# Optimization experiments

Hardware: AMD Instinct MI355X
Metric: run time of the kernel (lower is better)

## Reference

```python
import jax, jax.numpy as jnp
import numpy as np

ALPHA = 0.2          # LeakyReLU negative slope
ORTHO_LAMBDA = 0.01  # orthogonal regularization weight


def setup_inputs() -> dict:
    key = jax.random.key(0)
    ks = jax.random.split(key, 9)
    N, IN, OUT, NR, H = 50000, 128, 128, 64, 4
    E1, E2 = 200000, 50000
    return {
        "input": jax.random.normal(ks[0], (N, IN), jnp.float32),
        "edge": jax.random.randint(ks[1], (2, E1), 0, N),
        "edge_embed": jax.random.normal(ks[2], (E1, NR), jnp.float32),
        "edge_list_nhop": jax.random.randint(ks[3], (2, E2), 0, N),
        "edge_embed_nhop": jax.random.normal(ks[4], (E2, NR), jnp.float32),
        "proj": jax.random.normal(ks[5], (H, IN, IN), jnp.float32) / np.sqrt(IN).astype(np.float32),
        "W": jax.random.normal(ks[6], (H, OUT, 2 * IN + NR), jnp.float32) * 0.08,
        "a": jax.random.normal(ks[7], (H, 1, OUT), jnp.float32) * 0.1,
        "head_weights": jnp.ones((H,), jnp.float32),
    }


def reference(input, edge, edge_embed, edge_list_nhop, edge_embed_nhop, proj, W, a, head_weights):
    N, IN = input.shape
    H, OUT, _ = W.shape
    e = jnp.concatenate([edge, edge_list_nhop], axis=1)              # [2, E]
    emb = jnp.concatenate([edge_embed, edge_embed_nhop], axis=0)     # [E, NR]
    src, tgt = e[0], e[1]

    # per-head orthogonal projections: head_input[h] = input @ proj[h].T -> [H, N, IN]
    hin = jnp.einsum('ni,hoi->hno', input, proj)

    # edge_m = W @ concat(h_src, h_tgt, rel) without materializing the concat
    W_src, W_tgt, W_rel = W[:, :, :IN], W[:, :, IN:2 * IN], W[:, :, 2 * IN:]
    edge_m = (jnp.einsum('hei,hoi->heo', hin[:, src, :], W_src)
              + jnp.einsum('hei,hoi->heo', hin[:, tgt, :], W_tgt)
              + jnp.einsum('er,hor->heo', emb, W_rel))               # [H, E, OUT]

    scores = jnp.einsum('heo,ho->he', edge_m, a[:, 0, :])            # [H, E]
    powers = -jnp.where(scores > 0, scores, ALPHA * scores)         # -leakyrelu
    edge_e = jnp.exp(powers)                                         # [H, E]

    seg = lambda v: jax.ops.segment_sum(v, src, num_segments=N)
    e_rowsum = jnp.clip(jax.vmap(seg)(edge_e), 1e-12, None)          # [H, N]

    edge_w = edge_e[:, :, None] * edge_m                             # [H, E, OUT]
    head_out = jax.vmap(seg)(edge_w)                                 # [H, N, OUT]

    w = jax.nn.softmax(head_weights)
    out = jnp.einsum('h,hnd->nd', w, head_out)                       # [N, OUT]
    # faithful to torch: divides by the LAST head's e_rowsum (loop leakage)
    out = out / e_rowsum[-1][:, None]

    pp = jnp.einsum('hij,hkj->hik', proj, proj)                      # proj @ proj.T
    eye = jnp.eye(proj.shape[1], dtype=proj.dtype)
    orth_reg = ORTHO_LAMBDA * jnp.sum(jnp.sqrt(jnp.sum((pp - eye) ** 2, axis=(1, 2))))

    return jax.nn.elu(out), orth_reg
```

## Files before the change

kernel.cpp:

```cpp
#include <hip/hip_runtime.h>
#include <math.h>


#define NHEAD 4

typedef unsigned short u16;
typedef __attribute__((ext_vector_type(4))) unsigned short u16x4;
typedef __attribute__((ext_vector_type(8))) unsigned short u16x8;
typedef __attribute__((ext_vector_type(8))) short bf16x8;
typedef __attribute__((ext_vector_type(4))) float f32x4;

__device__ __forceinline__ float bf2f(u16 v) {
    union { unsigned u; float f; } x; x.u = ((unsigned)v) << 16; return x.f;
}
__device__ __forceinline__ u16 f2bf(float f) {
    union { float f; unsigned u; } x; x.f = f;
    const unsigned r = x.u + 0x7FFFu + ((x.u >> 16) & 1u);
    return (u16)(r >> 16);
}

__global__ __launch_bounds__(256) void k1_prep(
    const float* __restrict__ proj, const float* __restrict__ W,
    const float* __restrict__ a, const float* __restrict__ hw,
    u16* __restrict__ M_bf,
    float* __restrict__ asrc, float* __restrict__ atgt, float* __restrict__ arel,
    u16* __restrict__ WcatT_bf, float* __restrict__ wsoft,
    float* __restrict__ orth_part)
{
    __shared__ float projS[128*132];
    __shared__ float WS[32*132];
    __shared__ float tS[128];
    __shared__ float red[256];
    const int h = blockIdx.x;
    const int part = blockIdx.y;
    const int z = blockIdx.z;
    const int tid = threadIdx.x;
    if (part < 2 && z >= 4) return;
    const float* projH = proj + h*(128*128);
    const float* WH = W + h*(128*320);
    const float* aH = a + h*128;

    {
        const float4* p4 = (const float4*)projH;
        for (int idx = tid; idx < 4096; idx += 256)
            *(float4*)&projS[(idx>>5)*132 + (idx&31)*4] = p4[idx];
    }

    if (part < 2) {
        const int koff = part ? 128 : 0;
        for (int idx = tid; idx < 1024; idx += 256) {
            const int ol = idx>>5, jq = idx&31;
            *(float4*)&WS[ol*132 + jq*4] = *(const float4*)&WH[(z*32+ol)*320 + koff + jq*4];
        }
        __syncthreads();
        u16* Mout = M_bf + ((size_t)(part*4 + h))*16384;
        for (int idx = tid; idx < 1024; idx += 256) {
            const int ol = idx>>5, jq = idx&31;
            float4 acc; acc.x=0.f; acc.y=0.f; acc.z=0.f; acc.w=0.f;
            for (int i = 0; i < 128; ++i) {
                const float wv = WS[ol*132 + i];
                const float4 pv = *(const float4*)&projS[i*132 + jq*4];
                acc.x += wv*pv.x; acc.y += wv*pv.y; acc.z += wv*pv.z; acc.w += wv*pv.w;
            }
            u16x4 pk; pk.x=f2bf(acc.x); pk.y=f2bf(acc.y); pk.z=f2bf(acc.z); pk.w=f2bf(acc.w);
            *(u16x4*)&Mout[(z*32+ol)*128 + jq*4] = pk;
        }
        if (z == 0) {
            if (tid < 128) {
                float s = 0.f;
                for (int o = 0; o < 128; ++o) s += aH[o]*WH[o*320 + koff + tid];
                tS[tid] = s;
            }
            __syncthreads();
            if (tid < 128) {
                float s = 0.f;
                for (int i = 0; i < 128; ++i) s += tS[i]*projS[i*132 + tid];
                (part ? atgt : asrc)[h*128 + tid] = s;
            }
        }
    } else {
        __syncthreads();
        float local = 0.f;
        const int base = z*2048;
        for (int idx = base + tid; idx < base + 2048; idx += 256) {
            const int i = idx>>7, k = idx&127;
            if (i > k) continue;
            float s = 0.f;
            for (int q = 0; q < 32; ++q) {
                const float4 pi = *(const float4*)&projS[i*132 + q*4];
                const float4 pk = *(const float4*)&projS[k*132 + q*4];
                s += pi.x*pk.x + pi.y*pk.y + pi.z*pk.z + pi.w*pk.w;
            }
            if (i == k) { s -= 1.f; local += s*s; }
            else local += 2.f*s*s;
        }
        red[tid] = local;
        __syncthreads();
        for (int st = 128; st > 0; st >>= 1) {
            if (tid < st) red[tid] += red[tid+st];
            __syncthreads();
        }
        if (tid == 0) atomicAdd(&orth_part[h], red[0]);
        if (z == 0) {
            if (tid < 64) {
                float s = 0.f;
                for (int o = 0; o < 128; ++o) s += aH[o]*WH[o*320 + 256 + tid];
                arel[h*64 + tid] = s;
            }
            for (int idx = tid; idx < 8192; idx += 256) {
                const int r = idx & 63, o = idx >> 6;
                WcatT_bf[(size_t)o*256 + h*64 + r] = f2bf(WH[o*320 + 256 + r]);
            }
            if (h == 0 && tid == 0) {
                const float m = fmaxf(fmaxf(hw[0],hw[1]), fmaxf(hw[2],hw[3]));
                const float e0=expf(hw[0]-m), e1=expf(hw[1]-m), e2=expf(hw[2]-m), e3=expf(hw[3]-m);
                const float s = e0+e1+e2+e3;
                wsoft[0]=e0/s; wsoft[1]=e1/s; wsoft[2]=e2/s; wsoft[3]=e3/s;
            }
        }
    }
}

__global__ __launch_bounds__(256) void k0_nodes(
    const float* __restrict__ input, const float* __restrict__ asrc, const float* __restrict__ atgt,
    const int* __restrict__ edge, const int* __restrict__ nhop,
    u16* __restrict__ in_bf, float* __restrict__ s_src, float* __restrict__ s_tgt,
    int* __restrict__ deg, int N, int E1, int E2)
{
    __shared__ float aS[512], tS[512];
    const int tid = threadIdx.x;
    for (int idx = tid; idx < 512; idx += 256) { aS[idx] = asrc[idx]; tS[idx] = atgt[idx]; }
    const int t = blockIdx.x*256 + tid;
    if (t < E1 + E2) {
        const int src = (t < E1) ? edge[t] : nhop[t-E1];
        atomicAdd(&deg[src], 1);
    }
    __syncthreads();
    const int n = t;
    if (n >= N) return;
    const float4* inr = (const float4*)(input + (size_t)n*128);
    u16* ob = in_bf + (size_t)n*128;
    float ss[4] = {0.f,0.f,0.f,0.f}, st[4] = {0.f,0.f,0.f,0.f};
    for (int q = 0; q < 32; ++q) {
        const float4 v = inr[q];
        u16x4 pk; pk.x=f2bf(v.x); pk.y=f2bf(v.y); pk.z=f2bf(v.z); pk.w=f2bf(v.w);
        *(u16x4*)(ob + q*4) = pk;
        #pragma unroll
        for (int hh = 0; hh < 4; ++hh) {
            const float4 av = *(const float4*)&aS[hh*128 + q*4];
            const float4 tv = *(const float4*)&tS[hh*128 + q*4];
            ss[hh] += v.x*av.x + v.y*av.y + v.z*av.z + v.w*av.w;
            st[hh] += v.x*tv.x + v.y*tv.y + v.z*tv.z + v.w*tv.w;
        }
    }
    float4 o1; o1.x=ss[0]; o1.y=ss[1]; o1.z=ss[2]; o1.w=ss[3];
    float4 o2; o2.x=st[0]; o2.y=st[1]; o2.z=st[2]; o2.w=st[3];
    *(float4*)(s_src + (size_t)n*4) = o1;
    *(float4*)(s_tgt + (size_t)n*4) = o2;
}

__global__ __launch_bounds__(256) void k2_mfma(
    const u16* __restrict__ in_bf, const u16* __restrict__ M_bf,
    u16* __restrict__ tbl, int N)
{
    __shared__ u16 MS[16384];
    __shared__ u16 DW[4][16*136];
    const int tid = threadIdx.x;
    const int w = tid >> 6, lane = tid & 63;
    const int bid = blockIdx.x;
    const int chunk = gridDim.x >> 3;
    const int swz = (bid & 7)*chunk + (bid >> 3);
    const int n0 = (swz >> 2)*256;
    const int mat = swz & 3;
    const int m = lane & 15, kg = lane >> 4;

    {
        const u16* Mp = M_bf + (size_t)(4 + mat)*16384;
        for (int c = tid; c < 2048; c += 256) {
            const int row = c >> 4, c16 = c & 15;
            const u16x8 v = *(const u16x8*)(Mp + row*128 + c16*8);
            *(u16x8*)((char*)MS + row*256 + ((c16*16) ^ ((row&7)<<4))) = v;
        }
    }
    __syncthreads();

    bf16x8 fa[8][4];
    #pragma unroll
    for (int nt = 0; nt < 8; ++nt) {
        const int row = nt*16 + m;
        #pragma unroll
        for (int ks = 0; ks < 4; ++ks) {
            const int c16 = ks*4 + kg;
            fa[nt][ks] = *(const bf16x8*)((const char*)MS + row*256 + ((c16*16) ^ ((row&7)<<4)));
        }
    }

    for (int sub = 0; sub < 4; ++sub) {
        const int nrow = n0 + w*64 + sub*16 + m;
        const int nclamp = (nrow < N) ? nrow : (N-1);
        bf16x8 fb[4];
        #pragma unroll
        for (int ks = 0; ks < 4; ++ks)
            fb[ks] = *(const bf16x8*)(in_bf + (size_t)nclamp*128 + ks*32 + kg*8);
        f32x4 acc[8];
        #pragma unroll
        for (int nt = 0; nt < 8; ++nt) { acc[nt][0]=0.f; acc[nt][1]=0.f; acc[nt][2]=0.f; acc[nt][3]=0.f; }
        #pragma unroll
        for (int nt = 0; nt < 8; ++nt)
            #pragma unroll
            for (int ks = 0; ks < 4; ++ks)
                acc[nt] = __builtin_amdgcn_mfma_f32_16x16x32_bf16(fa[nt][ks], fb[ks], acc[nt], 0, 0, 0);
        #pragma unroll
        for (int nt = 0; nt < 8; ++nt) {
            unsigned lo, hi;
            asm("v_cvt_pk_bf16_f32 %0, %1, %2" : "=v"(lo) : "v"(acc[nt][0]), "v"(acc[nt][1]));
            asm("v_cvt_pk_bf16_f32 %0, %1, %2" : "=v"(hi) : "v"(acc[nt][2]), "v"(acc[nt][3]));
            uint2 pk; pk.x = lo; pk.y = hi;
            *(uint2*)&DW[w][m*136 + nt*16 + kg*4] = pk;
        }
        const int nb = n0 + w*64 + sub*16;
        #pragma unroll
        for (int k = 0; k < 4; ++k) {
            const int idx = lane + k*64;
            const int row = idx >> 4, seg = idx & 15;
            const int n = nb + row;
            if (n < N) {
                const bf16x8 v = *(const bf16x8*)&DW[w][row*136 + seg*8];
                *(bf16x8*)(tbl + (size_t)n*512 + mat*128 + seg*8) = v;
            }
        }
    }
}

__global__ __launch_bounds__(1024) void k_scanA(const int* __restrict__ deg, int* __restrict__ offsets,
                                                int* __restrict__ bsum, int* __restrict__ boff,
                                                int* __restrict__ sdone, int N, int nb)
{
    __shared__ int wsumS[16];
    __shared__ int ticketS;
    const int tid = threadIdx.x;
    const int lane = tid & 63, wid = tid >> 6;
    const int i0 = blockIdx.x*4096 + tid*4;
    int a0=0,a1=0,a2=0,a3=0;
    if (i0 + 3 < N) { const int4 t = *(const int4*)(deg + i0); a0=t.x; a1=t.y; a2=t.z; a3=t.w; }
    else { if (i0 < N) a0=deg[i0]; if (i0+1 < N) a1=deg[i0+1]; if (i0+2 < N) a2=deg[i0+2]; }
    const int s1=a0+a1, s2=s1+a2, s3=s2+a3;
    int s = s3;
    #pragma unroll
    for (int d = 1; d < 64; d <<= 1) { const int t = __shfl_up(s, d); if (lane >= d) s += t; }
    if (lane == 63) wsumS[wid] = s;
    __syncthreads();
    if (tid < 16) {
        int t = wsumS[tid];
        #pragma unroll
        for (int d = 1; d < 16; d <<= 1) { const int u = __shfl_up(t, d); if (tid >= d) t += u; }
        wsumS[tid] = t;
    }
    __syncthreads();
    const int ex = (wid ? wsumS[wid-1] : 0) + s - s3;
    if (i0 < N)     offsets[i0]   = ex;
    if (i0+1 < N)   offsets[i0+1] = ex + a0;
    if (i0+2 < N)   offsets[i0+2] = ex + s1;
    if (i0+3 < N)   offsets[i0+3] = ex + s2;
    if (tid == 0) {
        bsum[blockIdx.x] = wsumS[15];
        __threadfence();
        ticketS = atomicAdd(sdone, 1);
    }
    __syncthreads();
    if (ticketS == nb - 1 && tid < 64) {
        const int v = (tid < nb) ? atomicAdd(&bsum[tid], 0) : 0;
        int sv = v;
        #pragma unroll
        for (int d = 1; d < 64; d <<= 1) { const int t = __shfl_up(sv, d); if (tid >= d) sv += t; }
        if (tid < nb) boff[tid] = sv - v;
        if (tid == 63) offsets[N] = sv;
    }
}

__global__ __launch_bounds__(256) void k_fill2(
    const int* __restrict__ edge, const int* __restrict__ nhop,
    const float* __restrict__ emb1, const float* __restrict__ emb2,
    const float* __restrict__ s_src, const float* __restrict__ s_tgt,
    const float* __restrict__ arel,
    const int* __restrict__ offsets, const int* __restrict__ boff, int* __restrict__ cursor,
    int* __restrict__ csr_tgt, float* __restrict__ ee_perm, u16* __restrict__ emb_perm,
    int E1, int E2)
{
    __shared__ u16 embS[256*64];
    __shared__ float scS[256][4];
    __shared__ int pS[256];
    const int tid = threadIdx.x;
    const int g = tid >> 4, l = tid & 15;
    const int E = E1 + E2;
    const int ebase = blockIdx.x*256;

    {
        const float4 ar0 = *(const float4*)(arel + 0*64 + l*4);
        const float4 ar1 = *(const float4*)(arel + 1*64 + l*4);
        const float4 ar2 = *(const float4*)(arel + 2*64 + l*4);
        const float4 ar3 = *(const float4*)(arel + 3*64 + l*4);
        #pragma unroll 4
        for (int it = 0; it < 16; ++it) {
            const int el = it*16 + g;
            const int e = ebase + el;
            if (e >= E) continue;
            const float4 v = (e < E1) ? *(const float4*)(emb1 + (size_t)e*64 + l*4)
                                      : *(const float4*)(emb2 + (size_t)(e-E1)*64 + l*4);
            u16x4 pk; pk.x=f2bf(v.x); pk.y=f2bf(v.y); pk.z=f2bf(v.z); pk.w=f2bf(v.w);
            *(u16x4*)&embS[el*64 + l*4] = pk;
            float p0 = v.x*ar0.x + v.y*ar0.y + v.z*ar0.z + v.w*ar0.w;
            float p1 = v.x*ar1.x + v.y*ar1.y + v.z*ar1.z + v.w*ar1.w;
            float p2 = v.x*ar2.x + v.y*ar2.y + v.z*ar2.z + v.w*ar2.w;
            float p3 = v.x*ar3.x + v.y*ar3.y + v.z*ar3.z + v.w*ar3.w;
            #pragma unroll
            for (int d = 1; d < 16; d <<= 1) {
                p0 += __shfl_xor(p0, d);
                p1 += __shfl_xor(p1, d);
                p2 += __shfl_xor(p2, d);
                p3 += __shfl_xor(p3, d);
            }
            if (l == 0) {
                float4 sc; sc.x=p0; sc.y=p1; sc.z=p2; sc.w=p3;
                *(float4*)&scS[el][0] = sc;
            }
        }
    }
    __syncthreads();

    {
        const int e = ebase + tid;
        if (e < E) {
            int src, tgt;
            if (e < E1) { src = edge[e]; tgt = edge[E1+e]; }
            else { const int e2 = e-E1; src = nhop[e2]; tgt = nhop[E2+e2]; }
            const float4 s4 = *(const float4*)(s_src + (size_t)src*4);
            const float4 t4 = *(const float4*)(s_tgt + (size_t)tgt*4);
            const float4 pr = *(const float4*)&scS[tid][0];
            float4 eo;
            { const float sc = s4.x+t4.x+pr.x; eo.x = expf(sc>0.f ? -sc : -0.2f*sc); }
            { const float sc = s4.y+t4.y+pr.y; eo.y = expf(sc>0.f ? -sc : -0.2f*sc); }
            { const float sc = s4.z+t4.z+pr.z; eo.z = expf(sc>0.f ? -sc : -0.2f*sc); }
            { const float sc = s4.w+t4.w+pr.w; eo.w = expf(sc>0.f ? -sc : -0.2f*sc); }
            const int pos = atomicAdd(&cursor[src], 1);
            const int p = offsets[src] + boff[src>>12] + pos;
            csr_tgt[p] = tgt;
            *(float4*)(ee_perm + (size_t)p*4) = eo;
            pS[tid] = p;
        }
    }
    __syncthreads();

    #pragma unroll 4
    for (int it = 0; it < 16; ++it) {
        const int el = it*16 + g;
        const int e = ebase + el;
        if (e >= E) continue;
        const int p = pS[el];
        const u16x4 pk = *(const u16x4*)&embS[el*64 + l*4];
        *(u16x4*)(emb_perm + (size_t)p*64 + l*4) = pk;
    }
}

__global__ __launch_bounds__(256) void k4_gather(
    const float* __restrict__ ee_perm, const int* __restrict__ offsets, const int* __restrict__ boff,
    const int* __restrict__ csr_tgt,
    const u16* __restrict__ emb_perm, const u16* __restrict__ tbl,
    const float* __restrict__ wsoft,
    u16* __restrict__ pout_bf, u16* __restrict__ semb_bf, float* __restrict__ rowsum4,
    int N)
{
    __shared__ float eeS[4][64][4];
    __shared__ int   tgS[4][64];
    const int lane = threadIdx.x & 63;
    const int wv = threadIdx.x >> 6;
    const int n = blockIdx.x*4 + wv;
    if (n >= N) return;
    const int hl = lane >> 4;
    const int hoff = hl*128 + (lane & 15)*8;

    union HT { u16x8 v; unsigned u[4]; };

    float acc[8];
    #pragma unroll
    for (int j = 0; j < 8; ++j) acc[j] = 0.f;
    float sm0=0.f, sm1=0.f, sm2=0.f, sm3=0.f;
    float rsl0=0.f, rsl1=0.f, rsl2=0.f, rsl3=0.f;

    const int start = offsets[n] + boff[n>>12];
    const int end = (n+1 == N) ? offsets[N] : (offsets[n+1] + boff[(n+1)>>12]);
    for (int cb = start; cb < end; cb += 64) {
        const int rem = end - cb;
        const int cnt = rem < 64 ? rem : 64;
        int tgtL = 0;
        float4 eeL; eeL.x=0.f; eeL.y=0.f; eeL.z=0.f; eeL.w=0.f;
        if (lane < cnt) {
            tgtL = csr_tgt[cb + lane];
            eeL  = *(const float4*)(ee_perm + (size_t)(cb + lane)*4);
        }
        rsl0 += eeL.x; rsl1 += eeL.y; rsl2 += eeL.z; rsl3 += eeL.w;
        *(float4*)&eeS[wv][lane][0] = eeL;
        tgS[wv][lane] = tgtL;
        const int cp = (cnt + 3) & ~3;

        HT zz; zz.u[0]=0u; zz.u[1]=0u; zz.u[2]=0u; zz.u[3]=0u;
        HT ht0=zz, ht1=zz, ht2=zz, ht3=zz;
        u16 em0=0, em1=0, em2=0, em3=0;
#define K4_FETCH(J, IDX) { const int tg_ = tgS[wv][IDX]; \
            ht##J.v = *(const u16x8*)(tbl + (size_t)tg_*512 + hoff); \
            em##J = emb_perm[(size_t)(cb + (IDX))*64 + lane]; }
        if (0 < cnt) K4_FETCH(0, 0)
        if (1 < cnt) K4_FETCH(1, 1)
        if (2 < cnt) K4_FETCH(2, 2)
        if (3 < cnt) K4_FETCH(3, 3)

#define K4_STAGE(J) { \
            const float4 ee4 = *(const float4*)&eeS[wv][i+J][0]; \
            const float eh = eeS[wv][i+J][hl]; \
            _Pragma("unroll") \
            for (int p = 0; p < 4; ++p) { \
                union{unsigned u; float f;} lo_, hi_; \
                lo_.u = ht##J.u[p] << 16; hi_.u = ht##J.u[p] & 0xffff0000u; \
                acc[2*p]   += eh*lo_.f; \
                acc[2*p+1] += eh*hi_.f; \
            } \
            const float ev = bf2f(em##J); \
            sm0 += ee4.x*ev; sm1 += ee4.y*ev; sm2 += ee4.z*ev; sm3 += ee4.w*ev; \
            { const int ii = i + 4 + J; if (ii < cnt) K4_FETCH(J, ii) } }

        for (int i = 0; i < cp; i += 4) {
            K4_STAGE(0)
            K4_STAGE(1)
            K4_STAGE(2)
            K4_STAGE(3)
        }
#undef K4_STAGE
#undef K4_FETCH
    }

    #pragma unroll
    for (int d = 1; d < 64; d <<= 1) {
        rsl0 += __shfl_xor(rsl0, d);
        rsl1 += __shfl_xor(rsl1, d);
        rsl2 += __shfl_xor(rsl2, d);
        rsl3 += __shfl_xor(rsl3, d);
    }
    if (lane == 0) {
        float4 r4; r4.x=rsl0; r4.y=rsl1; r4.z=rsl2; r4.w=rsl3;
        *(float4*)(rowsum4 + (size_t)n*4) = r4;
    }

    const float4 ws4 = *(const float4*)wsoft;
    const float wh = (hl==0)?ws4.x:(hl==1)?ws4.y:(hl==2)?ws4.z:ws4.w;
    float p[8];
    #pragma unroll
    for (int j = 0; j < 8; ++j) {
        float pv = wh*acc[j];
        pv += __shfl_xor(pv, 16);
        pv += __shfl_xor(pv, 32);
        p[j] = pv;
    }
    if (hl == 0) {
        u16 pk[8];
        #pragma unroll
        for (int j = 0; j < 8; ++j) pk[j] = f2bf(p[j]);
        *(u16x8*)(pout_bf + (size_t)n*128 + (lane & 15)*8) = *(u16x8*)pk;
    }
    u16* so = semb_bf + (size_t)n*256;
    so[lane]       = f2bf(ws4.x*sm0);
    so[64 + lane]  = f2bf(ws4.y*sm1);
    so[128 + lane] = f2bf(ws4.z*sm2);
    so[192 + lane] = f2bf(ws4.w*sm3);
}

__global__ __launch_bounds__(256) void k5_gemm(
    const u16* __restrict__ semb_bf, const u16* __restrict__ wcatT_bf,
    const u16* __restrict__ M_bf, const u16* __restrict__ in_bf,
    const u16* __restrict__ pout_bf,
    const float* __restrict__ rowsum4, const float* __restrict__ wsoft,
    const float* __restrict__ orth_part,
    float* __restrict__ out, int N)
{
    __shared__ __align__(16) char smemU[4*16*132*4];
    u16* MS = (u16*)smemU;
    float* DWbase = (float*)smemU;
    const int tid = threadIdx.x;
    if (blockIdx.x == 0 && tid == 0)
        out[(size_t)N*128] = 0.01f*(sqrtf(orth_part[0])+sqrtf(orth_part[1])+sqrtf(orth_part[2])+sqrtf(orth_part[3]));
    const int w = tid >> 6, lane = tid & 63;
    const int m = lane & 15, kg = lane >> 4;
    const int n0 = blockIdx.x*128;

    const float4 ws4 = *(const float4*)wsoft;
    int rowS[2];
    float4 rhS[2];
    #pragma unroll
    for (int sub = 0; sub < 2; ++sub) {
        int r = n0 + w*32 + sub*16 + m; if (r >= N) r = N-1;
        rowS[sub] = r;
        const float4 rs = *(const float4*)(rowsum4 + (size_t)r*4);
        rhS[sub].x = ws4.x*rs.x; rhS[sub].y = ws4.y*rs.y;
        rhS[sub].z = ws4.z*rs.z; rhS[sub].w = ws4.w*rs.w;
    }

    f32x4 acc[2][8];
    #pragma unroll
    for (int sub = 0; sub < 2; ++sub)
        #pragma unroll
        for (int nt = 0; nt < 8; ++nt) { acc[sub][nt][0]=0.f; acc[sub][nt][1]=0.f; acc[sub][nt][2]=0.f; acc[sub][nt][3]=0.f; }

    #pragma unroll
    for (int half = 0; half < 2; ++half) {
        __syncthreads();
        for (int c = tid; c < 2048; c += 256) {
            const int r = c >> 4, c16 = c & 15;
            const u16x8 v = *(const u16x8*)(wcatT_bf + (size_t)r*256 + half*128 + c16*8);
            *(u16x8*)((char*)MS + r*256 + ((c16*16) ^ ((r&7)<<4))) = v;
        }
        __syncthreads();
        #pragma unroll
        for (int sub = 0; sub < 2; ++sub) {
            bf16x8 fa[4];
            const u16* ap = semb_bf + (size_t)rowS[sub]*256 + half*128 + kg*8;
            #pragma unroll
            for (int ks = 0; ks < 4; ++ks) fa[ks] = *(const bf16x8*)(ap + ks*32);
            #pragma unroll
            for (int nt = 0; nt < 8; ++nt) {
                const int o = nt*16 + m;
                #pragma unroll
                for (int ks = 0; ks < 4; ++ks) {
                    const int c16 = ks*4 + kg;
                    const bf16x8 fb = *(const bf16x8*)((const char*)MS + o*256 + ((c16*16) ^ ((o&7)<<4)));
                    acc[sub][nt] = __builtin_amdgcn_mfma_f32_16x16x32_bf16(fa[ks], fb, acc[sub][nt], 0, 0, 0);
                }
            }
        }
    }

    for (int h = 0; h < 4; ++h) {
        __syncthreads();
        {
            const u16* Mp = M_bf + (size_t)h*16384;
            for (int c = tid; c < 2048; c += 256) {
                const int r = c >> 4, c16 = c & 15;
                const u16x8 v = *(const u16x8*)(Mp + r*128 + c16*8);
                *(u16x8*)((char*)MS + r*256 + ((c16*16) ^ ((r&7)<<4))) = v;
            }
        }
        __syncthreads();
        #pragma unroll
        for (int sub = 0; sub < 2; ++sub) {
            const float rsc = (h==0)?rhS[sub].x:(h==1)?rhS[sub].y:(h==2)?rhS[sub].z:rhS[sub].w;
            union IU { bf16x8 v; unsigned u[4]; };
            bf16x8 fsc[4];
            const u16* ip = in_bf + (size_t)rowS[sub]*128 + kg*8;
            #pragma unroll
            for (int ks = 0; ks < 4; ++ks) {
                IU t; t.v = *(const bf16x8*)(ip + ks*32);
                IU o;
                #pragma unroll
                for (int p = 0; p < 4; ++p) {
                    union{unsigned u; float f;} lo_, hi_;
                    lo_.u = t.u[p] << 16; hi_.u = t.u[p] & 0xffff0000u;
                    const float a = lo_.f*rsc, b = hi_.f*rsc;
                    unsigned pk;
                    asm("v_cvt_pk_bf16_f32 %0, %1, %2" : "=v"(pk) : "v"(a), "v"(b));
                    o.u[p] = pk;
                }
                fsc[ks] = o.v;
            }
            #pragma unroll
            for (int nt = 0; nt < 8; ++nt) {
                const int o = nt*16 + m;
                #pragma unroll
                for (int ks = 0; ks < 4; ++ks) {
                    const int c16 = ks*4 + kg;
                    const bf16x8 fb = *(const bf16x8*)((const char*)MS + o*256 + ((c16*16) ^ ((o&7)<<4)));
                    acc[sub][nt] = __builtin_amdgcn_mfma_f32_16x16x32_bf16(fsc[ks], fb, acc[sub][nt], 0, 0, 0);
                }
            }
        }
    }

    __syncthreads();
    float* DW = DWbase + w*16*132;
    #pragma unroll
    for (int sub = 0; sub < 2; ++sub) {
        #pragma unroll
        for (int nt = 0; nt < 8; ++nt) {
            #pragma unroll
            for (int r = 0; r < 4; ++r)
                DW[(kg*4+r)*132 + nt*16 + m] = acc[sub][nt][r];
        }
        const int nb = n0 + w*32 + sub*16;
        #pragma unroll
        for (int k = 0; k < 8; ++k) {
            const int idx = lane + k*64;
            const int row = idx >> 5, q = idx & 31;
            const int n = nb + row;
            if (n < N) {
                const float4 d = *(const float4*)&DW[row*132 + q*4];
                const u16x4 pb = *(const u16x4*)(pout_bf + (size_t)n*128 + q*4);
                const float rinv = 1.0f / fmaxf(rowsum4[(size_t)n*4 + 3], 1e-12f);
                float v0 = (bf2f(pb.x) + d.x)*rinv;
                float v1 = (bf2f(pb.y) + d.y)*rinv;
                float v2 = (bf2f(pb.z) + d.z)*rinv;
                float v3 = (bf2f(pb.w) + d.w)*rinv;
                v0 = (v0 > 0.f) ? v0 : expm1f(v0);
                v1 = (v1 > 0.f) ? v1 : expm1f(v1);
                v2 = (v2 > 0.f) ? v2 : expm1f(v2);
                v3 = (v3 > 0.f) ? v3 : expm1f(v3);
                float4 r4; r4.x=v0; r4.y=v1; r4.z=v2; r4.w=v3;
                *(float4*)(out + (size_t)n*128 + q*4) = r4;
            }
        }
    }
}

extern "C" void kernel_launch(void* const* d_in, const int* in_sizes, int n_in,
                              void* d_out, int out_size, void* d_ws, size_t ws_size,
                              hipStream_t stream)
{
    const float* input = (const float*)d_in[0];
    const int*   edge  = (const int*)d_in[1];
    const float* emb1  = (const float*)d_in[2];
    const int*   nhop  = (const int*)d_in[3];
    const float* emb2  = (const float*)d_in[4];
    const float* proj  = (const float*)d_in[5];
    const float* W     = (const float*)d_in[6];
    const float* a     = (const float*)d_in[7];
    const float* hw    = (const float*)d_in[8];
    float* out = (float*)d_out;

    const int N  = in_sizes[0] / 128;
    const int E1 = in_sizes[1] / 2;
    const int E2 = in_sizes[3] / 2;
    const int E  = E1 + E2;
    (void)n_in; (void)out_size; (void)ws_size;

    char* wsb = (char*)d_ws;
    size_t off = 0;
    auto alloc = [&](size_t bytes) -> char* {
        char* p = wsb + off;
        off += (bytes + 255) & ~(size_t)255;
        return p;
    };
    u16*   in_bf    = (u16*)alloc((size_t)N*128*2);
    u16*   tbl      = (u16*)alloc((size_t)N*512*2);
    u16*   semb_bf  = (u16*)alloc((size_t)N*256*2);
    u16*   pout_bf  = (u16*)alloc((size_t)N*128*2);
    u16*   emb_perm = (u16*)alloc((size_t)E*64*2);
    float* ee_perm  = (float*)alloc((size_t)E*4*4);
    int*   csr_tgt  = (int*)alloc((size_t)E*4);
    u16*   M_bf     = (u16*)alloc((size_t)8*16384*2);
    u16*   WcatT_bf = (u16*)alloc((size_t)128*256*2);
    float* asrc     = (float*)alloc(512*4);
    float* atgt     = (float*)alloc(512*4);
    float* arel     = (float*)alloc(256*4);
    float* s_src    = (float*)alloc((size_t)N*4*4);
    float* s_tgt    = (float*)alloc((size_t)N*4*4);
    float* wsoft    = (float*)alloc(4*4);
    float* rowsum4  = (float*)alloc((size_t)N*4*4);
    int*   offsets  = (int*)alloc((size_t)(N+1)*4);
    int*   bsum     = (int*)alloc(64*4);
    int*   boff     = (int*)alloc(64*4);
    const size_t zoff0 = off;
    float* orth_part= (float*)alloc(4*4);
    int*   deg      = (int*)alloc((size_t)N*4);
    int*   cursor   = (int*)alloc((size_t)N*4);
    int*   sdone    = (int*)alloc(4);
    const size_t zoff1 = off;

    hipMemsetAsync(wsb + zoff0, 0, zoff1 - zoff0, stream);

    const int nbScan = (N + 4095) / 4096;
    const int nx = (N + 255) / 256;
    const int nx2 = (N + 127) / 128;
    const int nk0 = ((E > N ? E : N) + 255) / 256;

    k1_prep<<<dim3(NHEAD,3,8), dim3(256), 0, stream>>>(proj, W, a, hw, M_bf,
                                                       asrc, atgt, arel, WcatT_bf, wsoft, orth_part);
    k0_nodes<<<dim3(nk0), dim3(256), 0, stream>>>(input, asrc, atgt, edge, nhop,
                                                  in_bf, s_src, s_tgt, deg, N, E1, E2);
    k2_mfma<<<dim3(nx*4), dim3(256), 0, stream>>>(in_bf, M_bf, tbl, N);
    k_scanA<<<dim3(nbScan), dim3(1024), 0, stream>>>(deg, offsets, bsum, boff, sdone, N, nbScan);
    k_fill2<<<dim3((E+255)/256), dim3(256), 0, stream>>>(edge, nhop, emb1, emb2, s_src, s_tgt,
                                                         arel, offsets, boff, cursor,
                                                         csr_tgt, ee_perm, emb_perm, E1, E2);
    k4_gather<<<dim3((N+3)/4), dim3(256), 0, stream>>>(ee_perm, offsets, boff, csr_tgt, emb_perm,
                                                       tbl, wsoft, pout_bf, semb_bf, rowsum4, N);
    k5_gemm<<<dim3(nx2), dim3(256), 0, stream>>>(semb_bf, WcatT_bf, M_bf, in_bf, pout_bf,
                                                 rowsum4, wsoft, orth_part, out, N);
}
```

Baseline: 244.4 us.

## Precompute per-node source-side head tables in k2 instead of k5 GEMM

The per-head source-node contribution (input times M_h, scaled by rowsum) moves out of k5's MFMA loop. k2 now also computes the four source matrices, so it launches twice as many blocks and writes a separate bf16 table. k5 then reads that table in its epilogue and applies the rowsum weights as an elementwise FMA. This trades four in-k5 GEMM passes, which reloaded M into LDS each time, for an extra 100MB-scale write and read of the N×512 bf16 table, and rounds the partial result to bf16 before it is scaled.

```diff
diff --git a/kernel.cpp b/kernel.cpp
--- a/kernel.cpp
+++ b/kernel.cpp
@@ -161,7 +161,7 @@
 
 __global__ __launch_bounds__(256) void k2_mfma(
     const u16* __restrict__ in_bf, const u16* __restrict__ M_bf,
-    u16* __restrict__ tbl, int N)
+    u16* __restrict__ hsrc_tbl, u16* __restrict__ tbl, int N)
 {
     __shared__ u16 MS[16384];
     __shared__ u16 DW[4][16*136];
@@ -170,12 +170,12 @@
     const int bid = blockIdx.x;
     const int chunk = gridDim.x >> 3;
     const int swz = (bid & 7)*chunk + (bid >> 3);
-    const int n0 = (swz >> 2)*256;
-    const int mat = swz & 3;
+    const int n0 = (swz >> 3)*256;
+    const int mat = swz & 7;
     const int m = lane & 15, kg = lane >> 4;
 
     {
-        const u16* Mp = M_bf + (size_t)(4 + mat)*16384;
+        const u16* Mp = M_bf + (size_t)mat*16384;
         for (int c = tid; c < 2048; c += 256) {
             const int row = c >> 4, c16 = c & 15;
             const u16x8 v = *(const u16x8*)(Mp + row*128 + c16*8);
@@ -194,6 +194,8 @@
             fa[nt][ks] = *(const bf16x8*)((const char*)MS + row*256 + ((c16*16) ^ ((row&7)<<4)));
         }
     }
+
+    u16* outT = (mat < 4) ? (hsrc_tbl + mat*128) : (tbl + (mat-4)*128);
 
     for (int sub = 0; sub < 4; ++sub) {
         const int nrow = n0 + w*64 + sub*16 + m;
@@ -226,7 +228,7 @@
             const int n = nb + row;
             if (n < N) {
                 const bf16x8 v = *(const bf16x8*)&DW[w][row*136 + seg*8];
-                *(bf16x8*)(tbl + (size_t)n*512 + mat*128 + seg*8) = v;
+                *(bf16x8*)(outT + (size_t)n*512 + seg*8) = v;
             }
         }
     }
@@ -475,8 +477,7 @@
 
 __global__ __launch_bounds__(256) void k5_gemm(
     const u16* __restrict__ semb_bf, const u16* __restrict__ wcatT_bf,
-    const u16* __restrict__ M_bf, const u16* __restrict__ in_bf,
-    const u16* __restrict__ pout_bf,
+    const u16* __restrict__ hsrc_tbl, const u16* __restrict__ pout_bf,
     const float* __restrict__ rowsum4, const float* __restrict__ wsoft,
     const float* __restrict__ orth_part,
     float* __restrict__ out, int N)
@@ -490,17 +491,13 @@
     const int w = tid >> 6, lane = tid & 63;
     const int m = lane & 15, kg = lane >> 4;
     const int n0 = blockIdx.x*128;
-
     const float4 ws4 = *(const float4*)wsoft;
+
     int rowS[2];
-    float4 rhS[2];
     #pragma unroll
     for (int sub = 0; sub < 2; ++sub) {
         int r = n0 + w*32 + sub*16 + m; if (r >= N) r = N-1;
         rowS[sub] = r;
-        const float4 rs = *(const float4*)(rowsum4 + (size_t)r*4);
-        rhS[sub].x = ws4.x*rs.x; rhS[sub].y = ws4.y*rs.y;
-        rhS[sub].z = ws4.z*rs.z; rhS[sub].w = ws4.w*rs.w;
     }
 
     f32x4 acc[2][8];
@@ -537,51 +534,6 @@
         }
     }
 
-    for (int h = 0; h < 4; ++h) {
-        __syncthreads();
-        {
-            const u16* Mp = M_bf + (size_t)h*16384;
-            for (int c = tid; c < 2048; c += 256) {
-                const int r = c >> 4, c16 = c & 15;
-                const u16x8 v = *(const u16x8*)(Mp + r*128 + c16*8);
-                *(u16x8*)((char*)MS + r*256 + ((c16*16) ^ ((r&7)<<4))) = v;
-            }
-        }
-        __syncthreads();
-        #pragma unroll
-        for (int sub = 0; sub < 2; ++sub) {
-            const float rsc = (h==0)?rhS[sub].x:(h==1)?rhS[sub].y:(h==2)?rhS[sub].z:rhS[sub].w;
-            union IU { bf16x8 v; unsigned u[4]; };
-            bf16x8 fsc[4];
-            const u16* ip = in_bf + (size_t)rowS[sub]*128 + kg*8;
-            #pragma unroll
-            for (int ks = 0; ks < 4; ++ks) {
-                IU t; t.v = *(const bf16x8*)(ip + ks*32);
-                IU o;
-                #pragma unroll
-                for (int p = 0; p < 4; ++p) {
-                    union{unsigned u; float f;} lo_, hi_;
-                    lo_.u = t.u[p] << 16; hi_.u = t.u[p] & 0xffff0000u;
-                    const float a = lo_.f*rsc, b = hi_.f*rsc;
-                    unsigned pk;
-                    asm("v_cvt_pk_bf16_f32 %0, %1, %2" : "=v"(pk) : "v"(a), "v"(b));
-                    o.u[p] = pk;
-                }
-                fsc[ks] = o.v;
-            }
-            #pragma unroll
-            for (int nt = 0; nt < 8; ++nt) {
-                const int o = nt*16 + m;
-                #pragma unroll
-                for (int ks = 0; ks < 4; ++ks) {
-                    const int c16 = ks*4 + kg;
-                    const bf16x8 fb = *(const bf16x8*)((const char*)MS + o*256 + ((c16*16) ^ ((o&7)<<4)));
-                    acc[sub][nt] = __builtin_amdgcn_mfma_f32_16x16x32_bf16(fsc[ks], fb, acc[sub][nt], 0, 0, 0);
-                }
-            }
-        }
-    }
-
     __syncthreads();
     float* DW = DWbase + w*16*132;
     #pragma unroll
@@ -601,11 +553,18 @@
             if (n < N) {
                 const float4 d = *(const float4*)&DW[row*132 + q*4];
                 const u16x4 pb = *(const u16x4*)(pout_bf + (size_t)n*128 + q*4);
-                const float rinv = 1.0f / fmaxf(rowsum4[(size_t)n*4 + 3], 1e-12f);
-                float v0 = (bf2f(pb.x) + d.x)*rinv;
-                float v1 = (bf2f(pb.y) + d.y)*rinv;
-                float v2 = (bf2f(pb.z) + d.z)*rinv;
-                float v3 = (bf2f(pb.w) + d.w)*rinv;
+                const float4 rs = *(const float4*)(rowsum4 + (size_t)n*4);
+                const float rh0 = ws4.x*rs.x, rh1 = ws4.y*rs.y, rh2 = ws4.z*rs.z, rh3 = ws4.w*rs.w;
+                const u16* hp = hsrc_tbl + (size_t)n*512 + q*4;
+                const u16x4 h0 = *(const u16x4*)(hp);
+                const u16x4 h1 = *(const u16x4*)(hp + 128);
+                const u16x4 h2 = *(const u16x4*)(hp + 256);
+                const u16x4 h3 = *(const u16x4*)(hp + 384);
+                const float rinv = 1.0f / fmaxf(rs.w, 1e-12f);
+                float v0 = (bf2f(pb.x) + d.x + rh0*bf2f(h0.x) + rh1*bf2f(h1.x) + rh2*bf2f(h2.x) + rh3*bf2f(h3.x))*rinv;
+                float v1 = (bf2f(pb.y) + d.y + rh0*bf2f(h0.y) + rh1*bf2f(h1.y) + rh2*bf2f(h2.y) + rh3*bf2f(h3.y))*rinv;
+                float v2 = (bf2f(pb.z) + d.z + rh0*bf2f(h0.z) + rh1*bf2f(h1.z) + rh2*bf2f(h2.z) + rh3*bf2f(h3.z))*rinv;
+                float v3 = (bf2f(pb.w) + d.w + rh0*bf2f(h0.w) + rh1*bf2f(h1.w) + rh2*bf2f(h2.w) + rh3*bf2f(h3.w))*rinv;
                 v0 = (v0 > 0.f) ? v0 : expm1f(v0);
                 v1 = (v1 > 0.f) ? v1 : expm1f(v1);
                 v2 = (v2 > 0.f) ? v2 : expm1f(v2);
@@ -647,6 +606,7 @@
     };
     u16*   in_bf    = (u16*)alloc((size_t)N*128*2);
     u16*   tbl      = (u16*)alloc((size_t)N*512*2);
+    u16*   hsrc_tbl = (u16*)alloc((size_t)N*512*2);
     u16*   semb_bf  = (u16*)alloc((size_t)N*256*2);
     u16*   pout_bf  = (u16*)alloc((size_t)N*128*2);
     u16*   emb_perm = (u16*)alloc((size_t)E*64*2);
@@ -682,13 +642,13 @@
                                                        asrc, atgt, arel, WcatT_bf, wsoft, orth_part);
     k0_nodes<<<dim3(nk0), dim3(256), 0, stream>>>(input, asrc, atgt, edge, nhop,
                                                   in_bf, s_src, s_tgt, deg, N, E1, E2);
-    k2_mfma<<<dim3(nx*4), dim3(256), 0, stream>>>(in_bf, M_bf, tbl, N);
+    k2_mfma<<<dim3(nx*8), dim3(256), 0, stream>>>(in_bf, M_bf, hsrc_tbl, tbl, N);
     k_scanA<<<dim3(nbScan), dim3(1024), 0, stream>>>(deg, offsets, bsum, boff, sdone, N, nbScan);
     k_fill2<<<dim3((E+255)/256), dim3(256), 0, stream>>>(edge, nhop, emb1, emb2, s_src, s_tgt,
                                                          arel, offsets, boff, cursor,
                                                          csr_tgt, ee_perm, emb_perm, E1, E2);
     k4_gather<<<dim3((N+3)/4), dim3(256), 0, stream>>>(ee_perm, offsets, boff, csr_tgt, emb_perm,
                                                        tbl, wsoft, pout_bf, semb_bf, rowsum4, N);
-    k5_gemm<<<dim3(nx2), dim3(256), 0, stream>>>(semb_bf, WcatT_bf, M_bf, in_bf, pout_bf,
+    k5_gemm<<<dim3(nx2), dim3(256), 0, stream>>>(semb_bf, WcatT_bf, hsrc_tbl, pout_bf,
                                                  rowsum4, wsoft, orth_part, out, N);
 }
```

Measured after the change: 228.4 us. 1.07x faster.
